# Kernel tuning notes

Measured on AMD Instinct MI355X. Metric: run time of the kernel, lower is better.

## Reference

```python
import jax, jax.numpy as jnp
import numpy as np

B, N, FH, H, FO = 8, 1024, 128, 8, 64
FIN = 2 * FH  # f_hid * 2
NEG = -1e9
SLOPE = 0.2  # leaky_relu negative slope (GAT default)


def setup_inputs() -> dict:
    key = jax.random.key(0)
    ks = jax.random.split(key, 10)
    x = jax.random.normal(ks[0], (B, FIN), jnp.float32)
    A = jax.random.randint(ks[1], (B, N, N), 0, 2, jnp.int32)  # 0/1 dense adjacency
    mask_zero = jnp.ones((B, N, 1), jnp.float32)  # node validity mask
    p_atten = jax.random.uniform(ks[2], (B, N), jnp.float32)  # unused in forward body
    e_atten = jax.random.uniform(ks[3], (B, N, FIN), jnp.float32)
    Npost = jax.random.normal(ks[4], (N, FIN), jnp.float32) * np.float32(1.0 / np.sqrt(FIN))  # kaiming-ish
    w = jax.random.normal(ks[5], (H, FIN, FO), jnp.float32) * np.float32(1.0 / np.sqrt(FIN))
    a_src = jax.random.normal(ks[6], (H, FO), jnp.float32) * np.float32(0.1)
    a_dst = jax.random.normal(ks[7], (H, FO), jnp.float32) * np.float32(0.1)
    bias = jnp.zeros((FO,), jnp.float32)
    return {"x": x, "A": A, "mask_zero": mask_zero, "p_atten": p_atten,
            "e_atten": e_atten, "Npost": Npost, "w": w, "a_src": a_src,
            "a_dst": a_dst, "bias": bias}


def reference(x, A, mask_zero, p_atten, e_atten, Npost, w, a_src, a_dst, bias):
    # broadcast-mul feature gating: x [B,FIN] repeated over N posts, gated by Npost*e_atten
    recx = x[:, None, :] * (Npost[None, :, :] * e_atten)          # [B,N,FIN]
    # BatchGAT (DeepInf-style multi-head graph attention, dropout disabled / eval mode)
    h = jnp.einsum('bnf,hfo->bhno', recx, w)                      # [B,H,N,FO]
    s = jnp.einsum('bhno,ho->bhn', h, a_src)                      # src attention term
    d = jnp.einsum('bhno,ho->bhn', h, a_dst)                      # dst attention term
    logits = jax.nn.leaky_relu(s[:, :, :, None] + d[:, :, None, :], SLOPE)  # [B,H,N,N]
    adj = (A > 0)[:, None, :, :]                                  # [B,1,N,N]
    logits = jnp.where(adj, logits, NEG)
    attn = jax.nn.softmax(logits, axis=-1)                        # masked row softmax
    out = jnp.einsum('bhnm,bhmo->bhno', attn, h) + bias           # aggregate neighbors
    out = out.mean(axis=1)                                        # average heads -> [B,N,FO]
    return out * mask_zero                                        # zero padded nodes
```

## Files before the change

kernel.cpp:

```cpp
#include <hip/hip_runtime.h>

typedef __attribute__((ext_vector_type(8))) short          bf16x8;
typedef __attribute__((ext_vector_type(8))) unsigned short u16x8;
typedef __attribute__((ext_vector_type(4))) unsigned short u16x4;
typedef __attribute__((ext_vector_type(4))) float          f32x4;
typedef __attribute__((ext_vector_type(4))) int            i32x4;
typedef __attribute__((ext_vector_type(4))) unsigned int   u32x4;

union U8 { u16x8 u; bf16x8 b; u32x4 w; };
union U4 { u16x4 u; unsigned w[2]; };

__device__ __forceinline__ unsigned short f2bf(float f){
  unsigned u = __float_as_uint(f);
  return (unsigned short)((u + 0x7fffu + ((u >> 16) & 1u)) >> 16);
}
__device__ __forceinline__ unsigned pack_bf16(float lo, float hi){
  unsigned a = __float_as_uint(hi) + 0x8000u;
  unsigned b = __float_as_uint(lo) + 0x8000u;
  return __builtin_amdgcn_perm(a, b, 0x07060302u);
}

#define NN  1024
#define FIN 256
#define NH  8
#define FO  64

__global__ __launch_bounds__(256) void stage0(
    const float* __restrict__ w, const int* __restrict__ A,
    const float* __restrict__ bias, const float* __restrict__ mz,
    unsigned short* __restrict__ wfrag, unsigned long long* __restrict__ Abits,
    float* __restrict__ out)
{
  const int tid = blockIdx.x * 256 + threadIdx.x;
  if (tid < 16384){
    const int lane = tid & 63, ss = (tid >> 6) & 3, kc = (tid >> 8) & 7, h = tid >> 11;
    const int o = 16 * ss + (lane & 15);
    const int f = kc * 32 + (lane >> 4) * 8;
    u16x8 r;
    #pragma unroll
    for (int j = 0; j < 8; j++) r[j] = f2bf(w[(h * FIN + f + j) * FO + o]);
    *(u16x8*)(wfrag + tid * 8) = r;
  }
  #pragma unroll
  for (int k = 0; k < 2; k++){
    const int i = tid + k * 262144;
    out[i] = bias[i & 63] * mz[i >> 6];
  }
  for (int i = tid; i < 8388608; i += 262144){
    unsigned long long m = __ballot(A[i] > 0);
    if ((threadIdx.x & 63) == 0) Abits[i >> 6] = m;
  }
}

__global__ __launch_bounds__(512, 4) void stageA(
    const float* __restrict__ x, const float* __restrict__ e_at,
    const float* __restrict__ Np, const unsigned short* __restrict__ wfrag,
    const float* __restrict__ a_src, const float* __restrict__ a_dst,
    unsigned short* __restrict__ hT,
    float* __restrict__ exps, float* __restrict__ exps2,
    float* __restrict__ expd, float* __restrict__ expd2)
{
  __shared__ unsigned short rex[16 * 264];
  const int t = threadIdx.x;
  const int n0 = blockIdx.x * 16, b = blockIdx.y;

  {
    const int row = t >> 5, f0 = (t & 31) * 8;
    const int nrow = n0 + row;
    const float* ep = e_at + (b * NN + nrow) * FIN + f0;
    const float* qp = Np + nrow * FIN + f0;
    const float* xp = x + b * FIN + f0;
    f32x4 e0 = *(const f32x4*)ep, e1 = *(const f32x4*)(ep + 4);
    f32x4 q0 = *(const f32x4*)qp, q1 = *(const f32x4*)(qp + 4);
    f32x4 x0 = *(const f32x4*)xp, x1 = *(const f32x4*)(xp + 4);
    u16x8 r;
    #pragma unroll
    for (int j = 0; j < 4; j++){
      r[j]     = f2bf(e0[j] * q0[j] * x0[j]);
      r[j + 4] = f2bf(e1[j] * q1[j] * x1[j]);
    }
    *(u16x8*)(rex + row * 264 + f0) = r;
  }
  __syncthreads();

  const int h = t >> 6, lane = t & 63, quad = lane >> 4, l15 = lane & 15;
  const unsigned short* wf = wfrag + h * 16384 + lane * 8;

  f32x4 acc[4] = {};
  #pragma unroll
  for (int kc = 0; kc < 8; kc++){
    U8 a0, bf[4];
    a0.u = *(const u16x8*)(rex + l15 * 264 + kc * 32 + quad * 8);
    #pragma unroll
    for (int ss = 0; ss < 4; ss++) bf[ss].u = *(const u16x8*)(wf + (kc * 4 + ss) * 512);
    #pragma unroll
    for (int ss = 0; ss < 4; ss++)
      acc[ss] = __builtin_amdgcn_mfma_f32_16x16x32_bf16(a0.b, bf[ss].b, acc[ss], 0, 0, 0);
  }

  {
    const int mtile = blockIdx.x >> 1, moff = (blockIdx.x & 1) * 16;
    unsigned short* pan = hT + (size_t)(((b * NH + h) * 32 + mtile) * 64) * 32;
    #pragma unroll
    for (int ss = 0; ss < 4; ss++){
      U4 v;
      v.w[0] = pack_bf16(acc[ss][0], acc[ss][1]);
      v.w[1] = pack_bf16(acc[ss][2], acc[ss][3]);
      *(u16x4*)(pan + (16 * ss + l15) * 32 + moff + quad * 4) = v.u;
    }
  }

  float as4[4], ad4[4];
  #pragma unroll
  for (int ss = 0; ss < 4; ss++){
    as4[ss] = a_src[h * FO + 16 * ss + l15];
    ad4[ss] = a_dst[h * FO + 16 * ss + l15];
  }
  #pragma unroll
  for (int i = 0; i < 4; i++){
    float ps = 0.f, pd = 0.f;
    #pragma unroll
    for (int ss = 0; ss < 4; ss++){ ps += acc[ss][i] * as4[ss]; pd += acc[ss][i] * ad4[ss]; }
    #pragma unroll
    for (int off = 1; off < 16; off <<= 1){
      ps += __shfl_xor(ps, off);
      pd += __shfl_xor(pd, off);
    }
    if (l15 == 0){
      const int idx = (b * NH + h) * NN + n0 + quad * 4 + i;
      exps [idx] = __expf(ps);
      exps2[idx] = __expf(0.2f * ps);
      expd [idx] = __expf(pd);
      expd2[idx] = __expf(0.2f * pd);
    }
  }
}

__global__ __launch_bounds__(512, 8) void stageB(
    const unsigned* __restrict__ Aw,
    const unsigned short* __restrict__ hT,
    const float* __restrict__ exps, const float* __restrict__ exps2,
    const float* __restrict__ expd, const float* __restrict__ expd2,
    const float* __restrict__ mz, float* __restrict__ out)
{
  __shared__ float ed_l[2 * NN];
  __shared__ float e2_l[2 * NN];
  __shared__ unsigned mask_l[32 * 33];
  __shared__ float l_l[4 * 16];
  const int t = threadIdx.x;

  const int id  = blockIdx.x;
  const int xcd = id & 7;
  const int rest = id >> 3;
  const int j   = rest & 31;
  const int p   = (rest >> 5) * 8 + xcd;
  const int n0  = j * 32;
  const int hq  = p & 3;
  const int b   = p >> 2;

  const int w = t >> 6, lane = t & 63, quad = lane >> 4, l15 = lane & 15;
  const int hl = w & 1, rg = (w >> 1) & 1, mh = w >> 2;
  const int h = hq * 2 + hl;

  if (t < 64) l_l[t] = 0.f;
  {
    const float* s1 = expd  + (b * NH + hq * 2) * NN;
    const float* s2 = expd2 + (b * NH + hq * 2) * NN;
    *(f32x4*)(ed_l + t * 4) = *(const f32x4*)(s1 + t * 4);
    *(f32x4*)(e2_l + t * 4) = *(const f32x4*)(s2 + t * 4);
  }
  #pragma unroll
  for (int k = 0; k < 2; k++){
    const int i = t + k * 512;
    mask_l[(i >> 5) * 33 + (i & 31)] = Aw[(b * NN + n0 + (i >> 5)) * 32 + (i & 31)];
  }
  __syncthreads();

  const int hb = (b * NH + h) * NN;
  const float Es  = exps [hb + n0 + rg * 16 + l15];
  const float Es2 = exps2[hb + n0 + rg * 16 + l15];
  const unsigned short* pb = hT + (size_t)(b * NH + h) * 65536 + l15 * 32 + quad * 8;
  const float* edh = ed_l + hl * NN + quad * 8;
  const float* e2h = e2_l + hl * NN + quad * 8;
  const unsigned* maskp = mask_l + (rg * 16 + l15) * 33;
  const int c0 = mh * 16;

  U8 pan[4];
  #pragma unroll
  for (int ss = 0; ss < 4; ss++)
    pan[ss].u = *(const u16x8*)(pb + (size_t)c0 * 2048 + ss * 512);

  f32x4 acc[4] = {};
  float lp = 0.f;

  for (int cc = 0; cc < 16; cc++){
    const int c = c0 + cc;
    const unsigned am = maskp[c] >> (quad * 8);
    float pv[8];
    #pragma unroll
    for (int g2 = 0; g2 < 2; g2++){
      f32x4 dv = *(const f32x4*)(edh + c * 32 + g2 * 4);
      f32x4 gv = *(const f32x4*)(e2h + c * 32 + g2 * 4);
      #pragma unroll
      for (int jj = 0; jj < 4; jj++){
        float e = fmaxf(Es * dv[jj], Es2 * gv[jj]);
        pv[g2 * 4 + jj] = (am & (1u << (g2 * 4 + jj))) ? e : 0.f;
      }
    }
    lp += ((pv[0] + pv[1]) + (pv[2] + pv[3])) + ((pv[4] + pv[5]) + (pv[6] + pv[7]));
    U8 pk;
    #pragma unroll
    for (int r = 0; r < 4; r++) pk.w[r] = pack_bf16(pv[2 * r], pv[2 * r + 1]);
    #pragma unroll
    for (int ss = 0; ss < 4; ss++)
      acc[ss] = __builtin_amdgcn_mfma_f32_16x16x32_bf16(pk.b, pan[ss].b, acc[ss], 0, 0, 0);
    if (cc + 1 < 16){
      #pragma unroll
      for (int ss = 0; ss < 4; ss++)
        pan[ss].u = *(const u16x8*)(pb + (size_t)(c + 1) * 2048 + ss * 512);
    }
  }

  lp += __shfl_xor(lp, 16);
  lp += __shfl_xor(lp, 32);
  if (lane < 16) atomicAdd(&l_l[(w & 3) * 16 + lane], lp);
  __syncthreads();

  const float* mzp = mz + b * NN + n0 + rg * 16;
  #pragma unroll
  for (int i = 0; i < 4; i++){
    const int row = quad * 4 + i;
    const float invm = (0.125f / l_l[(w & 3) * 16 + row]) * mzp[row];
    float* op = out + (size_t)(b * NN + n0 + rg * 16 + row) * FO + l15;
    #pragma unroll
    for (int ss = 0; ss < 4; ss++)
      atomicAdd(op + ss * 16, acc[ss][i] * invm);
  }
}

extern "C" void kernel_launch(void* const* d_in, const int* in_sizes, int n_in,
                              void* d_out, int out_size, void* d_ws, size_t ws_size,
                              hipStream_t stream)
{
  (void)in_sizes; (void)n_in; (void)out_size; (void)ws_size;
  const float* x    = (const float*)d_in[0];
  const int*   A    = (const int*)d_in[1];
  const float* mz   = (const float*)d_in[2];
  const float* e_at = (const float*)d_in[4];
  const float* Np   = (const float*)d_in[5];
  const float* w    = (const float*)d_in[6];
  const float* asrc = (const float*)d_in[7];
  const float* adst = (const float*)d_in[8];
  const float* bias = (const float*)d_in[9];
  float* out = (float*)d_out;

  char* ws = (char*)d_ws;
  unsigned short* wfrag = (unsigned short*)ws;
  unsigned short* hT    = (unsigned short*)(ws + 262144);
  float* exps  = (float*)(ws + 8650752);
  float* exps2 = (float*)(ws + 8912896);
  float* expd  = (float*)(ws + 9175040);
  float* expd2 = (float*)(ws + 9437184);
  unsigned long long* Abits = (unsigned long long*)(ws + 9699328);

  stage0<<<dim3(1024), dim3(256), 0, stream>>>(w, A, bias, mz, wfrag, Abits, out);
  stageA<<<dim3(64, 8), dim3(512), 0, stream>>>(x, e_at, Np, wfrag, asrc, adst,
                                                hT, exps, exps2, expd, expd2);
  stageB<<<dim3(1024), dim3(512), 0, stream>>>((const unsigned*)Abits, hT,
                                               exps, exps2, expd, expd2,
                                               mz, out);
}
```

Baseline: 170.7 us.

## Unroll adjacency packing, double-buffer panels, MFMA row sums, LDS-reduce output atomics

```diff
diff --git a/kernel.cpp b/kernel.cpp
--- a/kernel.cpp
+++ b/kernel.cpp
@@ -4,7 +4,6 @@
 typedef __attribute__((ext_vector_type(8))) unsigned short u16x8;
 typedef __attribute__((ext_vector_type(4))) unsigned short u16x4;
 typedef __attribute__((ext_vector_type(4))) float          f32x4;
-typedef __attribute__((ext_vector_type(4))) int            i32x4;
 typedef __attribute__((ext_vector_type(4))) unsigned int   u32x4;
 
 union U8 { u16x8 u; bf16x8 b; u32x4 w; };
@@ -46,9 +45,20 @@
     const int i = tid + k * 262144;
     out[i] = bias[i & 63] * mz[i >> 6];
   }
-  for (int i = tid; i < 8388608; i += 262144){
-    unsigned long long m = __ballot(A[i] > 0);
-    if ((threadIdx.x & 63) == 0) Abits[i >> 6] = m;
+  const int wid = tid >> 6, lane = threadIdx.x & 63;
+  #pragma unroll
+  for (int g = 0; g < 8; g++){
+    const int base = g * 1048576 + wid * 256;
+    const unsigned long long m0 = __ballot(A[base + lane] > 0);
+    const unsigned long long m1 = __ballot(A[base + 64 + lane] > 0);
+    const unsigned long long m2 = __ballot(A[base + 128 + lane] > 0);
+    const unsigned long long m3 = __ballot(A[base + 192 + lane] > 0);
+    if (lane == 0){
+      Abits[(base >> 6) + 0] = m0;
+      Abits[(base >> 6) + 1] = m1;
+      Abits[(base >> 6) + 2] = m2;
+      Abits[(base >> 6) + 3] = m3;
+    }
   }
 }
 
@@ -136,6 +146,30 @@
   }
 }
 
+#define BCHUNK(C, PAN)                                                          \
+  {                                                                             \
+    const int c_ = (C);                                                         \
+    const unsigned am_ = maskp[c_] >> (quad * 8);                               \
+    float pv_[8];                                                               \
+    _Pragma("unroll")                                                           \
+    for (int g2_ = 0; g2_ < 2; g2_++){                                          \
+      f32x4 dv_ = *(const f32x4*)(edh + c_ * 32 + g2_ * 4);                     \
+      f32x4 gv_ = *(const f32x4*)(e2h + c_ * 32 + g2_ * 4);                     \
+      _Pragma("unroll")                                                         \
+      for (int jj_ = 0; jj_ < 4; jj_++){                                        \
+        const float e_ = fmaxf(Es * dv_[jj_], Es2 * gv_[jj_]);                  \
+        pv_[g2_ * 4 + jj_] = (am_ & (1u << (g2_ * 4 + jj_))) ? e_ : 0.f;        \
+      }                                                                         \
+    }                                                                           \
+    U8 pk_;                                                                     \
+    _Pragma("unroll")                                                           \
+    for (int r_ = 0; r_ < 4; r_++) pk_.w[r_] = pack_bf16(pv_[2 * r_], pv_[2 * r_ + 1]); \
+    _Pragma("unroll")                                                           \
+    for (int ss_ = 0; ss_ < 4; ss_++)                                           \
+      acc[ss_] = __builtin_amdgcn_mfma_f32_16x16x32_bf16(pk_.b, PAN[ss_].b, acc[ss_], 0, 0, 0); \
+    accs = __builtin_amdgcn_mfma_f32_16x16x32_bf16(pk_.b, ones.b, accs, 0, 0, 0); \
+  }
+
 __global__ __launch_bounds__(512, 8) void stageB(
     const unsigned* __restrict__ Aw,
     const unsigned short* __restrict__ hT,
@@ -146,7 +180,8 @@
   __shared__ float ed_l[2 * NN];
   __shared__ float e2_l[2 * NN];
   __shared__ unsigned mask_l[32 * 33];
-  __shared__ float l_l[4 * 16];
+  __shared__ float l_l[64];
+  __shared__ float oacc[32 * 65];
   const int t = threadIdx.x;
 
   const int id  = blockIdx.x;
@@ -163,6 +198,7 @@
   const int h = hq * 2 + hl;
 
   if (t < 64) l_l[t] = 0.f;
+  for (int i = t; i < 32 * 65; i += 512) oacc[i] = 0.f;
   {
     const float* s1 = expd  + (b * NH + hq * 2) * NN;
     const float* s2 = expd2 + (b * NH + hq * 2) * NN;
@@ -185,56 +221,55 @@
   const unsigned* maskp = mask_l + (rg * 16 + l15) * 33;
   const int c0 = mh * 16;
 
-  U8 pan[4];
-  #pragma unroll
-  for (int ss = 0; ss < 4; ss++)
-    pan[ss].u = *(const u16x8*)(pb + (size_t)c0 * 2048 + ss * 512);
-
-  f32x4 acc[4] = {};
-  float lp = 0.f;
-
-  for (int cc = 0; cc < 16; cc++){
-    const int c = c0 + cc;
-    const unsigned am = maskp[c] >> (quad * 8);
-    float pv[8];
-    #pragma unroll
-    for (int g2 = 0; g2 < 2; g2++){
-      f32x4 dv = *(const f32x4*)(edh + c * 32 + g2 * 4);
-      f32x4 gv = *(const f32x4*)(e2h + c * 32 + g2 * 4);
-      #pragma unroll
-      for (int jj = 0; jj < 4; jj++){
-        float e = fmaxf(Es * dv[jj], Es2 * gv[jj]);
-        pv[g2 * 4 + jj] = (am & (1u << (g2 * 4 + jj))) ? e : 0.f;
-      }
-    }
-    lp += ((pv[0] + pv[1]) + (pv[2] + pv[3])) + ((pv[4] + pv[5]) + (pv[6] + pv[7]));
-    U8 pk;
-    #pragma unroll
-    for (int r = 0; r < 4; r++) pk.w[r] = pack_bf16(pv[2 * r], pv[2 * r + 1]);
-    #pragma unroll
-    for (int ss = 0; ss < 4; ss++)
-      acc[ss] = __builtin_amdgcn_mfma_f32_16x16x32_bf16(pk.b, pan[ss].b, acc[ss], 0, 0, 0);
-    if (cc + 1 < 16){
+  U8 ones;
+  #pragma unroll
+  for (int jj = 0; jj < 8; jj++) ones.u[jj] = 0x3F80;
+
+  U8 pan0[4], pan1[4];
+  #pragma unroll
+  for (int ss = 0; ss < 4; ss++){
+    pan0[ss].u = *(const u16x8*)(pb + (size_t)c0 * 2048 + ss * 512);
+    pan1[ss].u = *(const u16x8*)(pb + (size_t)(c0 + 1) * 2048 + ss * 512);
+  }
+
+  f32x4 acc[4] = {}, accs = {};
+
+  for (int cc = 0; cc < 16; cc += 2){
+    BCHUNK(c0 + cc, pan0)
+    if (cc + 2 < 16){
       #pragma unroll
       for (int ss = 0; ss < 4; ss++)
-        pan[ss].u = *(const u16x8*)(pb + (size_t)(c + 1) * 2048 + ss * 512);
-    }
-  }
-
-  lp += __shfl_xor(lp, 16);
-  lp += __shfl_xor(lp, 32);
-  if (lane < 16) atomicAdd(&l_l[(w & 3) * 16 + lane], lp);
+        pan0[ss].u = *(const u16x8*)(pb + (size_t)(c0 + cc + 2) * 2048 + ss * 512);
+    }
+    BCHUNK(c0 + cc + 1, pan1)
+    if (cc + 3 < 16){
+      #pragma unroll
+      for (int ss = 0; ss < 4; ss++)
+        pan1[ss].u = *(const u16x8*)(pb + (size_t)(c0 + cc + 3) * 2048 + ss * 512);
+    }
+  }
+
+  if (l15 == 0){
+    #pragma unroll
+    for (int i = 0; i < 4; i++)
+      atomicAdd(&l_l[(w & 3) * 16 + quad * 4 + i], accs[i]);
+  }
   __syncthreads();
 
   const float* mzp = mz + b * NN + n0 + rg * 16;
   #pragma unroll
   for (int i = 0; i < 4; i++){
-    const int row = quad * 4 + i;
-    const float invm = (0.125f / l_l[(w & 3) * 16 + row]) * mzp[row];
-    float* op = out + (size_t)(b * NN + n0 + rg * 16 + row) * FO + l15;
+    const int r16 = quad * 4 + i;
+    const float invm = (0.125f / l_l[(w & 3) * 16 + r16]) * mzp[r16];
     #pragma unroll
     for (int ss = 0; ss < 4; ss++)
-      atomicAdd(op + ss * 16, acc[ss][i] * invm);
+      atomicAdd(&oacc[(rg * 16 + r16) * 65 + ss * 16 + l15], acc[ss][i] * invm);
+  }
+  __syncthreads();
+
+  for (int i = t; i < 2048; i += 512){
+    const int r = i >> 6, o = i & 63;
+    atomicAdd(out + (size_t)(b * NN + n0 + r) * FO + o, oacc[r * 65 + o]);
   }
 }
 
```

Result: slower. 185.7 us (+8.8%).
